# Kernel optimization log

Hardware: AMD Instinct MI355X
Metric: run time of the kernel (lower is better)

The kernel has to match this reference:

```python
import jax, jax.numpy as jnp
import numpy as np

EPS = 1e-5  # BatchNorm eps (torch default)
PAD = 1
K = 9  # 3x3 kernel points

def conv3x3(x, w, b):
    # x: [B,C,H,W], w: [O,C,3,3]
    y = jax.lax.conv_general_dilated(x, w, (1, 1), ((PAD, PAD), (PAD, PAD)),
                                     dimension_numbers=('NCHW', 'OIHW', 'NCHW'))
    return y + b[None, :, None, None]

def deform_conv2d(x, offset, mask, weight, bias):
    # Modulated deformable conv v2, stride 1, pad 1, 3x3 kernel.
    # x: [B,C,H,W]; offset: [B,2K,H,W] (first K = dy, last K = dx); mask: [B,K,H,W]
    B, C, H, W = x.shape
    ki, kj = jnp.meshgrid(jnp.arange(3), jnp.arange(3), indexing='ij')
    ki = ki.reshape(K).astype(x.dtype)
    kj = kj.reshape(K).astype(x.dtype)
    dy = offset[:, :K].transpose(0, 2, 3, 1)   # [B,H,W,K]
    dx = offset[:, K:].transpose(0, 2, 3, 1)
    m = mask.transpose(0, 2, 3, 1)             # [B,H,W,K]
    hs = jnp.arange(H, dtype=x.dtype)
    ws = jnp.arange(W, dtype=x.dtype)
    py = hs[None, :, None, None] - PAD + ki[None, None, None, :] + dy  # [B,H,W,K]
    px = ws[None, None, :, None] - PAD + kj[None, None, None, :] + dx
    y0 = jnp.floor(py)
    x0 = jnp.floor(px)
    wy1 = py - y0
    wx1 = px - x0
    wy0 = 1.0 - wy1
    wx0 = 1.0 - wx1

    def gather(yi, xi):
        valid = ((yi >= 0) & (yi < H) & (xi >= 0) & (xi < W)).astype(x.dtype)
        yc = jnp.clip(yi, 0, H - 1).astype(jnp.int32)
        xc = jnp.clip(xi, 0, W - 1).astype(jnp.int32)
        g = jax.vmap(lambda img, yb, xb: img[:, yb, xb])(x, yc, xc)  # [B,C,H,W,K]
        return g * valid[:, None]

    val = (gather(y0, x0) * (wy0 * wx0)[:, None]
           + gather(y0, x0 + 1.0) * (wy0 * wx1)[:, None]
           + gather(y0 + 1.0, x0) * (wy1 * wx0)[:, None]
           + gather(y0 + 1.0, x0 + 1.0) * (wy1 * wx1)[:, None])
    val = val * m[:, None]  # modulation
    out = jnp.einsum('bchwk,ock->bohw', val, weight.reshape(weight.shape[0], C, K))
    return out + bias[None, :, None, None]

def dcnv2(x, w_om, b_om, w, b, gamma, beta, mean, var):
    om = conv3x3(x, w_om, b_om)               # [B,27,H,W]
    o1, o2, mr = jnp.split(om, 3, axis=1)
    offset = jnp.concatenate([o1, o2], axis=1)  # [B,18,H,W]
    mask = jax.nn.sigmoid(mr)
    y = deform_conv2d(x, offset, mask, w, b)
    scale = (gamma / jnp.sqrt(var + EPS))[None, :, None, None]
    y = (y - mean[None, :, None, None]) * scale + beta[None, :, None, None]
    return jax.nn.silu(y)

def setup_inputs() -> dict:
    key = jax.random.key(0)
    ks = jax.random.split(key, 9)
    B, C, H, W = 4, 256, 128, 128
    C4 = C // 4
    return {
        'x': jax.random.normal(ks[0], (B, C, H, W), jnp.float32),
        'w': jax.random.normal(ks[1], (4, C4, C4, 3, 3), jnp.float32) * 0.05,
        'b': jax.random.normal(ks[2], (4, C4), jnp.float32) * 0.05,
        'w_om': jax.random.normal(ks[3], (4, 27, C4, 3, 3), jnp.float32) * 0.01,
        'b_om': jax.random.normal(ks[4], (4, 27), jnp.float32) * 0.01,
        'gamma': jax.random.normal(ks[5], (4, C4), jnp.float32) * 0.1 + 1.0,
        'beta': jax.random.normal(ks[6], (4, C4), jnp.float32) * 0.1,
        'mean': jax.random.normal(ks[7], (4, C4), jnp.float32) * 0.1,
        'var': jax.random.uniform(ks[8], (4, C4), jnp.float32, minval=0.5, maxval=1.5),
    }

def reference(x, w, b, w_om, b_om, gamma, beta, mean, var):
    B, C, H, W = x.shape
    C4 = C // 4
    # channel-split into 4 independent groups, vmap identical DCNv2 over groups
    xg = x.reshape(B, 4, C4, H, W).transpose(1, 0, 2, 3, 4)  # [4,B,C4,H,W]
    yg = jax.vmap(dcnv2)(xg, w_om, b_om, w, b, gamma, beta, mean, var)
    return yg.transpose(1, 0, 2, 3, 4).reshape(B, C, H, W)
```

## Files before the change

### kernel.cpp

```cpp
#include <hip/hip_runtime.h>
#include <math.h>

#define Hs 128
#define Ws 128
#define HWs 16384

typedef __attribute__((ext_vector_type(8))) short short8;
typedef __attribute__((ext_vector_type(8))) __bf16 bf16x8;
typedef __attribute__((ext_vector_type(4))) float f32x4;
typedef __attribute__((ext_vector_type(2))) float f32x2;

static __device__ __forceinline__ float bf2f(unsigned short u) {
    union { unsigned int i; float f; } v; v.i = ((unsigned int)u) << 16; return v.f;
}
static __device__ __forceinline__ unsigned short f2bf(float f) {
    unsigned int u = __builtin_bit_cast(unsigned int, f);
    return (unsigned short)((u + 0x7fffu + ((u >> 16) & 1u)) >> 16);
}
static __device__ __forceinline__ f32x4 mfma16(short8 a, short8 b, f32x4 c) {
    return __builtin_amdgcn_mfma_f32_16x16x32_bf16(
        __builtin_bit_cast(bf16x8, a), __builtin_bit_cast(bf16x8, b), c, 0, 0, 0);
}
static __device__ __forceinline__ f32x2 pk_mul(f32x2 a, f32x2 b) {
    f32x2 d;
    asm("v_pk_mul_f32 %0, %1, %2" : "=v"(d) : "v"(a), "v"(b));
    return d;
}
static __device__ __forceinline__ f32x2 pk_fma(f32x2 a, f32x2 b, f32x2 c) {
    f32x2 d;
    asm("v_pk_fma_f32 %0, %1, %2, %3" : "=v"(d) : "v"(a), "v"(b), "v"(c));
    return d;
}
static __device__ __forceinline__ unsigned int cvt_pk_bf16(float lo, float hi) {
    unsigned int d;
    asm("v_cvt_pk_bf16_f32 %0, %1, %2" : "=v"(d) : "v"(lo), "v"(hi));
    return d;
}
static __device__ __forceinline__ f32x2 bfpair(unsigned int u) {
    union { unsigned int i[2]; f32x2 f; } v;
    v.i[0] = u << 16;
    v.i[1] = u & 0xffff0000u;
    return v.f;
}
static __device__ __forceinline__ void barrier_lds_only() {
    asm volatile("s_waitcnt lgkmcnt(0)\n\ts_barrier" ::: "memory");
}

__global__ __launch_bounds__(256) void k_xt(const float* __restrict__ x,
                                            const float* __restrict__ w,
                                            const float* __restrict__ b,
                                            const float* __restrict__ w_om,
                                            const float* __restrict__ gamma,
                                            const float* __restrict__ beta,
                                            const float* __restrict__ mean,
                                            const float* __restrict__ var,
                                            unsigned short* __restrict__ xT,
                                            unsigned short* __restrict__ w2,
                                            unsigned short* __restrict__ wom2,
                                            float* __restrict__ scsh) {
    const int tid = threadIdx.x;
    const int f = blockIdx.y * 256 + blockIdx.x;
    if (f < 576) {
        int idx = f * 256 + tid;
        if (idx < 4 * 64 * 576) {
            int go = idx / 576;
            int ck = idx - go * 576;
            int k = ck >> 6, c = ck & 63;
            w2[idx] = f2bf(w[go * 576 + c * 9 + k]);
        }
        if (idx < 4 * 32 * 576) {
            int gj = idx / 576;
            int g = gj >> 5, j = gj & 31;
            int ck = idx - gj * 576;
            int k = ck >> 6, c = ck & 63;
            float v = (j < 27) ? w_om[(g * 27 + j) * 576 + c * 9 + k] : 0.f;
            wom2[idx] = f2bf(v);
        }
        if (idx < 256) {
            float sc = gamma[idx] * rsqrtf(var[idx] + 1e-5f);
            scsh[idx] = sc;
            scsh[256 + idx] = (b[idx] - mean[idx]) * sc + beta[idx];
        }
    }

    const int img = blockIdx.y;
    const int g = img >> 2, bb = img & 3;
    const int p0 = blockIdx.x * 64;
    __shared__ float t[64 * 65];

    const float* xg = x + (size_t)(bb * 256 + g * 64) * HWs + p0;
    const int l16 = tid & 15, grp = tid >> 4;
#pragma unroll
    for (int pass = 0; pass < 4; ++pass) {
        int c = pass * 16 + grp;
        float4 v = *(const float4*)(xg + (size_t)c * HWs + l16 * 4);
        float* tr = &t[c * 65 + l16 * 4];
        tr[0] = v.x; tr[1] = v.y; tr[2] = v.z; tr[3] = v.w;
    }
    __syncthreads();
    const int p = tid >> 2, c16 = (tid & 3) * 16;
    unsigned short* dst = xT + (size_t)img * HWs * 64 + (size_t)(p0 + p) * 64 + c16;
    unsigned int rr[8];
#pragma unroll
    for (int q = 0; q < 8; ++q)
        rr[q] = cvt_pk_bf16(t[(c16 + 2 * q) * 65 + p], t[(c16 + 2 * q + 1) * 65 + p]);
    *(uint4*)dst       = make_uint4(rr[0], rr[1], rr[2], rr[3]);
    *(uint4*)(dst + 8) = make_uint4(rr[4], rr[5], rr[6], rr[7]);
}

__global__ __launch_bounds__(256, 3) void k_off(const unsigned short* __restrict__ xT,
                                                const unsigned short* __restrict__ wom2,
                                                const float* __restrict__ b_om,
                                                float* __restrict__ om) {
    const int img = blockIdx.y;
    const int g = img >> 2;
    const int h = blockIdx.x;
    const int tid = threadIdx.x;
    const int lane = tid & 63, wv = tid >> 6;
    const int mt = wv & 1, nh = wv >> 1;
    const int m = lane & 15, q = lane >> 4;

    __shared__ unsigned short xrow[3 * 130 * 64];

    const unsigned short* xTi = xT + (size_t)img * HWs * 64;
    for (int i = tid; i < 3 * 130 * 8; i += 256) {
        int rr = i / 1040;
        int rem = i - rr * 1040;
        int px = rem >> 3, j = rem & 7;
        int gh = h + rr - 1, gw = px - 1;
        uint4 v = make_uint4(0, 0, 0, 0);
        if (gh >= 0 && gh < Hs && gw >= 0 && gw < Ws)
            v = *(const uint4*)(xTi + (size_t)(gh * Ws + gw) * 64 + j * 8);
        *(uint4*)&xrow[(rr * 130 + px) * 64 + (j ^ (px & 7)) * 8] = v;
    }

    short8 afrag[18];
    const unsigned short* wb = wom2 + (size_t)(g * 32 + mt * 16 + m) * 576 + q * 8;
#pragma unroll
    for (int t = 0; t < 18; ++t) afrag[t] = *(const short8*)(wb + t * 32);

    f32x4 acc[4];
#pragma unroll
    for (int t = 0; t < 4; ++t) acc[t] = (f32x4){0.f, 0.f, 0.f, 0.f};

    __syncthreads();

#pragma unroll
    for (int k = 0; k < 9; ++k) {
        const int ki = k / 3, kj = k - ki * 3;
#pragma unroll
        for (int s = 0; s < 2; ++s) {
#pragma unroll
            for (int t = 0; t < 4; ++t) {
                int px = (nh * 4 + t) * 16 + m + kj;
                int gran = (s * 4 + q) ^ (px & 7);
                short8 bfrag = *(const short8*)&xrow[(ki * 130 + px) * 64 + gran * 8];
                acc[t] = mfma16(afrag[k * 2 + s], bfrag, acc[t]);
            }
        }
    }

    float* omi = om + (size_t)img * 27 * HWs + h * Ws;
#pragma unroll
    for (int t = 0; t < 4; ++t) {
#pragma unroll
        for (int r = 0; r < 4; ++r) {
            int j = mt * 16 + q * 4 + r;
            if (j < 27) {
                float v = acc[t][r] + b_om[g * 27 + j];
                if (j >= 18) v = 1.f / (1.f + __expf(-v));
                omi[(size_t)j * HWs + (nh * 4 + t) * 16 + m] = v;
            }
        }
    }
}

__global__ __launch_bounds__(256, 2) void k_def(const unsigned short* __restrict__ xT,
                                                const float* __restrict__ om,
                                                const unsigned short* __restrict__ w2,
                                                const float* __restrict__ scsh,
                                                float* __restrict__ out) {
    const int img = blockIdx.y;
    const int g = img >> 2, bb = img & 3;
    const int p0 = blockIdx.x * 64;
    const int tid = threadIdx.x;
    const int lane = tid & 63, wv = tid >> 6;
    const int m = lane & 15, q = lane >> 4;

    __shared__ int   pO[4][576];
    __shared__ float pW[4][576];
    __shared__ unsigned short val[2][64 * 64];
    __shared__ float lsc[64], lsh[64];

    if (tid < 64) {
        lsc[tid] = scsh[g * 64 + tid];
        lsh[tid] = scsh[256 + g * 64 + tid];
    }

    const float* omg = om + (size_t)img * 27 * HWs;
    for (int idx = tid; idx < 576; idx += 256) {
        int k = idx >> 6, pp = idx & 63;
        int p = p0 + pp;
        int h = p >> 7, w = p & 127;
        float dy = omg[k * HWs + p];
        float dx = omg[(9 + k) * HWs + p];
        float mk = omg[(18 + k) * HWs + p];
        int ki = k / 3, kj = k - ki * 3;
        float py = (float)(h - 1 + ki) + dy;
        float px = (float)(w - 1 + kj) + dx;
        float fy = floorf(py), fx = floorf(px);
        float wy1 = py - fy, wx1 = px - fx;
        float wy0 = 1.f - wy1, wx0 = 1.f - wx1;
        int y0 = (int)fy, x0 = (int)fx, y1 = y0 + 1, x1 = x0 + 1;
        bool vy0 = (y0 >= 0) && (y0 < Hs), vy1 = (y1 >= 0) && (y1 < Hs);
        bool vx0 = (x0 >= 0) && (x0 < Ws), vx1 = (x1 >= 0) && (x1 < Ws);
        int cy0 = min(max(y0, 0), Hs - 1), cy1 = min(max(y1, 0), Hs - 1);
        int cx0 = min(max(x0, 0), Ws - 1), cx1 = min(max(x1, 0), Ws - 1);
        pO[0][idx] = cy0 * Ws + cx0;
        pO[1][idx] = cy0 * Ws + cx1;
        pO[2][idx] = cy1 * Ws + cx0;
        pO[3][idx] = cy1 * Ws + cx1;
        pW[0][idx] = (vy0 && vx0) ? wy0 * wx0 * mk : 0.f;
        pW[1][idx] = (vy0 && vx1) ? wy0 * wx1 * mk : 0.f;
        pW[2][idx] = (vy1 && vx0) ? wy1 * wx0 * mk : 0.f;
        pW[3][idx] = (vy1 && vx1) ? wy1 * wx1 * mk : 0.f;
    }

    f32x4 acc[4];
#pragma unroll
    for (int t = 0; t < 4; ++t) acc[t] = (f32x4){0.f, 0.f, 0.f, 0.f};

    const unsigned short* xTi = xT + (size_t)img * HWs * 64;
    const int p = tid >> 2, c4 = tid & 3;
    const int wr_sw = ((p >> 1) & 7) << 3;
    const int rd_sw = ((m >> 1) & 7) << 3;

    __syncthreads();

    short8 af[2][2];
    const unsigned short* wb = w2 + (size_t)(g * 64 + wv * 16 + m) * 576 + q * 8;
    auto fetchA = [&](int k, int bf) {
        af[bf][0] = *(const short8*)(wb + (k * 2 + 0) * 32);
        af[bf][1] = *(const short8*)(wb + (k * 2 + 1) * 32);
    };

    uint4 gth[2][8];
    float wfb[2][4];
    auto fetch = [&](int k, int bf) {
        const int kb = k * 64 + p;
        const int off0 = pO[0][kb], off1 = pO[1][kb], off2 = pO[2][kb], off3 = pO[3][kb];
        wfb[bf][0] = pW[0][kb]; wfb[bf][1] = pW[1][kb];
        wfb[bf][2] = pW[2][kb]; wfb[bf][3] = pW[3][kb];
        const unsigned short* s0 = xTi + (size_t)off0 * 64 + c4 * 16;
        const unsigned short* s1 = xTi + (size_t)off1 * 64 + c4 * 16;
        const unsigned short* s2 = xTi + (size_t)off2 * 64 + c4 * 16;
        const unsigned short* s3 = xTi + (size_t)off3 * 64 + c4 * 16;
        gth[bf][0] = *(const uint4*)(s0);
        gth[bf][1] = *(const uint4*)(s1);
        gth[bf][2] = *(const uint4*)(s2);
        gth[bf][3] = *(const uint4*)(s3);
        gth[bf][4] = *(const uint4*)(s0 + 8);
        gth[bf][5] = *(const uint4*)(s1 + 8);
        gth[bf][6] = *(const uint4*)(s2 + 8);
        gth[bf][7] = *(const uint4*)(s3 + 8);
    };
    fetch(0, 0);
    fetchA(0, 0);

#pragma unroll
    for (int k = 0; k < 9; ++k) {
        const int cb = k & 1, nb = cb ^ 1;
        if (k < 8) {
            fetch(k + 1, nb);
            fetchA(k + 1, nb);
        }
        unsigned short* vb = &val[cb][0];
        const float* wf = wfb[cb];
        f32x2 w0p = {wf[0], wf[0]}, w1p = {wf[1], wf[1]};
        f32x2 w2p = {wf[2], wf[2]}, w3p = {wf[3], wf[3]};
#pragma unroll
        for (int it = 0; it < 2; ++it) {
            const int oc8 = (2 * c4 + it) * 8;
            unsigned int rr[4];
#pragma unroll
            for (int e = 0; e < 4; ++e) {
                f32x2 x0 = bfpair(((const unsigned int*)&gth[cb][it * 4 + 0])[e]);
                f32x2 x1 = bfpair(((const unsigned int*)&gth[cb][it * 4 + 1])[e]);
                f32x2 x2 = bfpair(((const unsigned int*)&gth[cb][it * 4 + 2])[e]);
                f32x2 x3 = bfpair(((const unsigned int*)&gth[cb][it * 4 + 3])[e]);
                f32x2 a = pk_mul(x0, w0p);
                a = pk_fma(x1, w1p, a);
                a = pk_fma(x2, w2p, a);
                a = pk_fma(x3, w3p, a);
                rr[e] = cvt_pk_bf16(a[0], a[1]);
            }
            *(uint4*)&vb[p * 64 + (oc8 ^ wr_sw)] = make_uint4(rr[0], rr[1], rr[2], rr[3]);
        }
        barrier_lds_only();
        const unsigned short* vr = &val[cb][0];
#pragma unroll
        for (int s = 0; s < 2; ++s) {
#pragma unroll
            for (int t = 0; t < 4; ++t) {
                const int row = t * 16 + m;
                short8 bfrag = *(const short8*)&vr[row * 64 + ((s * 32 + q * 8) ^ rd_sw)];
                acc[t] = mfma16(af[cb][s], bfrag, acc[t]);
            }
        }
    }

    float* outg = out + ((size_t)bb * 256 + g * 64) * HWs + p0;
#pragma unroll
    for (int t = 0; t < 4; ++t) {
#pragma unroll
        for (int r = 0; r < 4; ++r) {
            int o = wv * 16 + q * 4 + r;
            float y = acc[t][r] * lsc[o] + lsh[o];
            outg[(size_t)o * HWs + t * 16 + m] = y / (1.f + __expf(-y));
        }
    }
}

extern "C" void kernel_launch(void* const* d_in, const int* in_sizes, int n_in,
                              void* d_out, int out_size, void* d_ws, size_t ws_size,
                              hipStream_t stream) {
    const float* x     = (const float*)d_in[0];
    const float* w     = (const float*)d_in[1];
    const float* b     = (const float*)d_in[2];
    const float* w_om  = (const float*)d_in[3];
    const float* b_om  = (const float*)d_in[4];
    const float* gamma = (const float*)d_in[5];
    const float* beta  = (const float*)d_in[6];
    const float* mean  = (const float*)d_in[7];
    const float* var   = (const float*)d_in[8];
    float* out = (float*)d_out;

    char* ws = (char*)d_ws;
    float* om            = (float*)ws;
    unsigned short* xT   = (unsigned short*)(ws + 28311552);
    unsigned short* w2   = (unsigned short*)(ws + 61865984);
    unsigned short* wom2 = (unsigned short*)(ws + 62160896);
    float* scsh          = (float*)(ws + 62308352);

    hipLaunchKernelGGL(k_xt, dim3(256, 16), dim3(256), 0, stream,
                       x, w, b, w_om, gamma, beta, mean, var, xT, w2, wom2, scsh);
    hipLaunchKernelGGL(k_off, dim3(128, 16), dim3(256), 0, stream, xT, wom2, b_om, om);
    hipLaunchKernelGGL(k_def, dim3(256, 16), dim3(256), 0, stream, xT, om, w2, scsh, out);
}
```

Measured before the change: 242.0 us.

## Fuse offset/mask convolution into deformable conv kernel via shared-memory tile

Removes the separate offset/mask conv kernel and computes the 27-channel offset/mask conv per 64-pixel half-row inside the deformable kernel. A 3x66 halo tile of bf16 input is staged in LDS and later reused as the double-buffered val buffer. This drops the om global write and read and one launch. In exchange the halo rows are reloaded per half-row and there is an extra block-wide sync. LDS use also grows, which may limit occupancy.

Result: slower. 255.4 us (+5.5%).

```diff
diff --git a/kernel.cpp b/kernel.cpp
--- a/kernel.cpp
+++ b/kernel.cpp
@@ -108,88 +108,25 @@
     *(uint4*)(dst + 8) = make_uint4(rr[4], rr[5], rr[6], rr[7]);
 }
 
-__global__ __launch_bounds__(256, 3) void k_off(const unsigned short* __restrict__ xT,
+__global__ __launch_bounds__(256, 2) void k_def(const unsigned short* __restrict__ xT,
                                                 const unsigned short* __restrict__ wom2,
                                                 const float* __restrict__ b_om,
-                                                float* __restrict__ om) {
-    const int img = blockIdx.y;
-    const int g = img >> 2;
-    const int h = blockIdx.x;
-    const int tid = threadIdx.x;
-    const int lane = tid & 63, wv = tid >> 6;
-    const int mt = wv & 1, nh = wv >> 1;
-    const int m = lane & 15, q = lane >> 4;
-
-    __shared__ unsigned short xrow[3 * 130 * 64];
-
-    const unsigned short* xTi = xT + (size_t)img * HWs * 64;
-    for (int i = tid; i < 3 * 130 * 8; i += 256) {
-        int rr = i / 1040;
-        int rem = i - rr * 1040;
-        int px = rem >> 3, j = rem & 7;
-        int gh = h + rr - 1, gw = px - 1;
-        uint4 v = make_uint4(0, 0, 0, 0);
-        if (gh >= 0 && gh < Hs && gw >= 0 && gw < Ws)
-            v = *(const uint4*)(xTi + (size_t)(gh * Ws + gw) * 64 + j * 8);
-        *(uint4*)&xrow[(rr * 130 + px) * 64 + (j ^ (px & 7)) * 8] = v;
-    }
-
-    short8 afrag[18];
-    const unsigned short* wb = wom2 + (size_t)(g * 32 + mt * 16 + m) * 576 + q * 8;
-#pragma unroll
-    for (int t = 0; t < 18; ++t) afrag[t] = *(const short8*)(wb + t * 32);
-
-    f32x4 acc[4];
-#pragma unroll
-    for (int t = 0; t < 4; ++t) acc[t] = (f32x4){0.f, 0.f, 0.f, 0.f};
-
-    __syncthreads();
-
-#pragma unroll
-    for (int k = 0; k < 9; ++k) {
-        const int ki = k / 3, kj = k - ki * 3;
-#pragma unroll
-        for (int s = 0; s < 2; ++s) {
-#pragma unroll
-            for (int t = 0; t < 4; ++t) {
-                int px = (nh * 4 + t) * 16 + m + kj;
-                int gran = (s * 4 + q) ^ (px & 7);
-                short8 bfrag = *(const short8*)&xrow[(ki * 130 + px) * 64 + gran * 8];
-                acc[t] = mfma16(afrag[k * 2 + s], bfrag, acc[t]);
-            }
-        }
-    }
-
-    float* omi = om + (size_t)img * 27 * HWs + h * Ws;
-#pragma unroll
-    for (int t = 0; t < 4; ++t) {
-#pragma unroll
-        for (int r = 0; r < 4; ++r) {
-            int j = mt * 16 + q * 4 + r;
-            if (j < 27) {
-                float v = acc[t][r] + b_om[g * 27 + j];
-                if (j >= 18) v = 1.f / (1.f + __expf(-v));
-                omi[(size_t)j * HWs + (nh * 4 + t) * 16 + m] = v;
-            }
-        }
-    }
-}
-
-__global__ __launch_bounds__(256, 2) void k_def(const unsigned short* __restrict__ xT,
-                                                const float* __restrict__ om,
                                                 const unsigned short* __restrict__ w2,
                                                 const float* __restrict__ scsh,
                                                 float* __restrict__ out) {
     const int img = blockIdx.y;
     const int g = img >> 2, bb = img & 3;
     const int p0 = blockIdx.x * 64;
+    const int hrow = blockIdx.x >> 1;
+    const int xh = (blockIdx.x & 1) << 6;
     const int tid = threadIdx.x;
     const int lane = tid & 63, wv = tid >> 6;
     const int m = lane & 15, q = lane >> 4;
 
+    __shared__ __align__(16) unsigned short xwv[3 * 66 * 64];
+    __shared__ float om_l[27 * 64];
     __shared__ int   pO[4][576];
     __shared__ float pW[4][576];
-    __shared__ unsigned short val[2][64 * 64];
     __shared__ float lsc[64], lsh[64];
 
     if (tid < 64) {
@@ -197,14 +134,70 @@
         lsh[tid] = scsh[256 + g * 64 + tid];
     }
 
-    const float* omg = om + (size_t)img * 27 * HWs;
+    const unsigned short* xTi = xT + (size_t)img * HWs * 64;
+
+    for (int i = tid; i < 3 * 66 * 8; i += 256) {
+        int r = i / 528;
+        int rem = i - r * 528;
+        int px = rem >> 3, j = rem & 7;
+        int gh = hrow + r - 1, gw = xh + px - 1;
+        uint4 v = make_uint4(0, 0, 0, 0);
+        if (gh >= 0 && gh < Hs && gw >= 0 && gw < Ws)
+            v = *(const uint4*)(xTi + (size_t)(gh * Ws + gw) * 64 + j * 8);
+        *(uint4*)&xwv[(r * 66 + px) * 64 + ((j ^ (px & 7)) * 8)] = v;
+    }
+
+    const int mt = wv & 1, ct2 = wv >> 1;
+    short8 aom[18];
+    {
+        const unsigned short* wbo = wom2 + (size_t)(g * 32 + mt * 16 + m) * 576 + q * 8;
+#pragma unroll
+        for (int t = 0; t < 18; ++t) aom[t] = *(const short8*)(wbo + t * 32);
+    }
+
+    __syncthreads();
+
+    {
+        f32x4 accO[2];
+#pragma unroll
+        for (int t = 0; t < 2; ++t) accO[t] = (f32x4){0.f, 0.f, 0.f, 0.f};
+#pragma unroll
+        for (int k = 0; k < 9; ++k) {
+            const int ki = k / 3, kj = k - ki * 3;
+#pragma unroll
+            for (int s = 0; s < 2; ++s) {
+#pragma unroll
+                for (int t = 0; t < 2; ++t) {
+                    int px = (ct2 * 2 + t) * 16 + m + kj;
+                    int gran = (s * 4 + q) ^ (px & 7);
+                    short8 bfrag = *(const short8*)&xwv[(ki * 66 + px) * 64 + gran * 8];
+                    accO[t] = mfma16(aom[k * 2 + s], bfrag, accO[t]);
+                }
+            }
+        }
+#pragma unroll
+        for (int t = 0; t < 2; ++t) {
+#pragma unroll
+            for (int r = 0; r < 4; ++r) {
+                int j = mt * 16 + q * 4 + r;
+                if (j < 27) {
+                    float v = accO[t][r] + b_om[g * 27 + j];
+                    if (j >= 18) v = 1.f / (1.f + __expf(-v));
+                    om_l[j * 64 + (ct2 * 2 + t) * 16 + m] = v;
+                }
+            }
+        }
+    }
+
+    __syncthreads();
+
     for (int idx = tid; idx < 576; idx += 256) {
         int k = idx >> 6, pp = idx & 63;
         int p = p0 + pp;
         int h = p >> 7, w = p & 127;
-        float dy = omg[k * HWs + p];
-        float dx = omg[(9 + k) * HWs + p];
-        float mk = omg[(18 + k) * HWs + p];
+        float dy = om_l[k * 64 + pp];
+        float dx = om_l[(9 + k) * 64 + pp];
+        float mk = om_l[(18 + k) * 64 + pp];
         int ki = k / 3, kj = k - ki * 3;
         float py = (float)(h - 1 + ki) + dy;
         float px = (float)(w - 1 + kj) + dx;
@@ -230,7 +223,6 @@
 #pragma unroll
     for (int t = 0; t < 4; ++t) acc[t] = (f32x4){0.f, 0.f, 0.f, 0.f};
 
-    const unsigned short* xTi = xT + (size_t)img * HWs * 64;
     const int p = tid >> 2, c4 = tid & 3;
     const int wr_sw = ((p >> 1) & 7) << 3;
     const int rd_sw = ((m >> 1) & 7) << 3;
@@ -274,7 +266,7 @@
             fetch(k + 1, nb);
             fetchA(k + 1, nb);
         }
-        unsigned short* vb = &val[cb][0];
+        unsigned short* vb = &xwv[cb * 4096];
         const float* wf = wfb[cb];
         f32x2 w0p = {wf[0], wf[0]}, w1p = {wf[1], wf[1]};
         f32x2 w2p = {wf[2], wf[2]}, w3p = {wf[3], wf[3]};
@@ -297,7 +289,7 @@
             *(uint4*)&vb[p * 64 + (oc8 ^ wr_sw)] = make_uint4(rr[0], rr[1], rr[2], rr[3]);
         }
         barrier_lds_only();
-        const unsigned short* vr = &val[cb][0];
+        const unsigned short* vr = &xwv[cb * 4096];
 #pragma unroll
         for (int s = 0; s < 2; ++s) {
 #pragma unroll
@@ -336,7 +328,6 @@
     float* out = (float*)d_out;
 
     char* ws = (char*)d_ws;
-    float* om            = (float*)ws;
     unsigned short* xT   = (unsigned short*)(ws + 28311552);
     unsigned short* w2   = (unsigned short*)(ws + 61865984);
     unsigned short* wom2 = (unsigned short*)(ws + 62160896);
@@ -344,6 +335,6 @@
 
     hipLaunchKernelGGL(k_xt, dim3(256, 16), dim3(256), 0, stream,
                        x, w, b, w_om, gamma, beta, mean, var, xT, w2, wom2, scsh);
-    hipLaunchKernelGGL(k_off, dim3(128, 16), dim3(256), 0, stream, xT, wom2, b_om, om);
-    hipLaunchKernelGGL(k_def, dim3(256, 16), dim3(256), 0, stream, xT, om, w2, scsh, out);
-}
+    hipLaunchKernelGGL(k_def, dim3(256, 16), dim3(256), 0, stream,
+                       xT, wom2, b_om, w2, scsh, out);
+}
```
